# Kernel optimization log

Measured on AMD Instinct MI355X. Metric: run time of the kernel, lower is better.

The kernel has to match this reference:

```python
import jax, jax.numpy as jnp
import numpy as np

STD = 0.01

def setup_inputs() -> dict:
    key = jax.random.key(0)
    k1, k2, k3 = jax.random.split(key, 3)
    B, T, D = 16, 4096, 512
    x = jax.random.normal(k1, (B, T, D), dtype=jnp.float32)
    att_W = jax.random.normal(k2, (D, D), dtype=jnp.float32) * STD
    att_v = jax.random.normal(k3, (D,), dtype=jnp.float32) * STD
    return {"x": x, "att_W": att_W, "att_v": att_v}

def reference(x, att_W, att_v):
    # additive attention scores: tanh(x @ W) @ v -> [B, T]
    y = jnp.tanh(jnp.einsum('btd,de->bte', x, att_W))
    scores = jnp.einsum('btd,d->bt', y, att_v)
    weights = jax.nn.softmax(scores, axis=-1)          # softmax over sequence
    out = jnp.einsum('bt,btd->bd', weights, x)         # weighted sum pooling
    return out.astype(jnp.float32)
```

## Files before the change

### kernel.cpp

```cpp
#include <hip/hip_runtime.h>
#include <hip/hip_bf16.h>
#include <math.h>

#define BB 16
#define TT 4096
#define DD 512
#define MM (BB*TT)

typedef __bf16 bf16x8 __attribute__((ext_vector_type(8)));
typedef float  f32x4  __attribute__((ext_vector_type(4)));

__device__ inline unsigned short f2bf(float f) {
    unsigned u = __builtin_bit_cast(unsigned, f) + 0x8000u;
    return (unsigned short)(u >> 16);
}

__device__ inline unsigned pack_bf16x2(float lo, float hi) {
    unsigned u0 = __builtin_bit_cast(unsigned, lo) + 0x8000u;
    unsigned u1 = __builtin_bit_cast(unsigned, hi) + 0x8000u;
    return __builtin_amdgcn_perm(u1, u0, 0x07060302);
}

__device__ inline float tanh_fast(float y) {
    float e = __expf(2.0f * y);
    return 1.0f - 2.0f * __builtin_amdgcn_rcpf(e + 1.0f);
}

__global__ void wb_kernel(const float* __restrict__ W, unsigned short* __restrict__ Wb) {
    int u = blockIdx.x * 256 + threadIdx.x;
    int lane = u & 63;
    int fid  = u >> 6;
    int ni = fid & 1;
    int s  = (fid >> 1) & 15;
    int p  = (fid >> 5) & 7;
    int h  = fid >> 8;
    int n  = h * 256 + p * 32 + ni * 16 + (lane & 15);
    int k0 = s * 32 + (lane >> 4) * 8;
    unsigned short o[8];
    #pragma unroll
    for (int j = 0; j < 8; j++) o[j] = f2bf(W[(size_t)(k0 + j) * DD + n]);
    *(uint4*)(Wb + (size_t)u * 8) = *(uint4*)o;
}

__global__ __launch_bounds__(512, 2) void scorepool_kernel(
        const float* __restrict__ x, const unsigned short* __restrict__ Wb,
        const float* __restrict__ v,
        float* __restrict__ num_ws, float* __restrict__ mz_ws) {
    __shared__ unsigned short As[64 * DD];
    __shared__ float sbuf[4][64];
    __shared__ float ew[64];
    __shared__ float mzsh[2];
    __shared__ float psum[4][DD];

    const int tid  = threadIdx.x;
    const int m0   = blockIdx.x * 64;
    const int wid  = tid >> 6;
    const int lane = tid & 63;
    const int l15  = lane & 15;
    const int q    = lane >> 4;
    const int r3   = l15 & 7;
    const int wr   = (wid & 1) * 32;
    const int wh   = wid >> 1;

    #pragma unroll 4
    for (int i = 0; i < 8; i++) {
        int u = i * 512 + tid;
        int r = u >> 6;
        int c = u & 63;
        const float* gp = x + (size_t)(m0 + r) * DD + c * 8;
        f32x4 f0 = __builtin_nontemporal_load((const f32x4*)(gp));
        f32x4 f1 = __builtin_nontemporal_load((const f32x4*)(gp + 4));
        uint4 o;
        o.x = pack_bf16x2(f0.x, f0.y);
        o.y = pack_bf16x2(f0.z, f0.w);
        o.z = pack_bf16x2(f1.x, f1.y);
        o.w = pack_bf16x2(f1.z, f1.w);
        *(uint4*)(&As[r * DD + (c ^ (r & 7)) * 8]) = o;
    }

    const unsigned short* bqp = Wb + (size_t)wh * 65536 + lane * 8;
    bf16x8 b[4][2];
    #pragma unroll
    for (int g = 0; g < 3; g++) {
        b[g][0] = *(const bf16x8*)(bqp);
        b[g][1] = *(const bf16x8*)(bqp + 512);
        bqp += 1024;
    }

    __syncthreads();

    float vpart[2][4];
    #pragma unroll
    for (int mi = 0; mi < 2; mi++)
        #pragma unroll
        for (int rr = 0; rr < 4; rr++)
            vpart[mi][rr] = 0.f;

#define A_FRAG(mi, s) (*(const bf16x8*)(&As[(wr + (mi)*16 + l15) * DD + ((((s)*4 + q) ^ r3) * 8)]))

    bf16x8 a[4][2];
    #pragma unroll
    for (int g = 0; g < 3; g++) {
        a[g][0] = A_FRAG(0, g);
        a[g][1] = A_FRAG(1, g);
    }

    #pragma unroll 1
    for (int p = 0; p < 4; p++) {
        f32x4 acc[2][2];
        #pragma unroll
        for (int mi = 0; mi < 2; mi++)
            #pragma unroll
            for (int ni = 0; ni < 2; ni++)
                acc[mi][ni] = (f32x4){0.f, 0.f, 0.f, 0.f};

        #pragma unroll
        for (int s = 0; s < 16; s++) {
            const int ns = (s + 3) & 15;
            a[(s + 3) & 3][0] = A_FRAG(0, ns);
            a[(s + 3) & 3][1] = A_FRAG(1, ns);
            b[(s + 3) & 3][0] = *(const bf16x8*)(bqp);
            b[(s + 3) & 3][1] = *(const bf16x8*)(bqp + 512);
            bqp += 1024;
            #pragma unroll
            for (int mi = 0; mi < 2; mi++)
                #pragma unroll
                for (int ni = 0; ni < 2; ni++)
                    acc[mi][ni] = __builtin_amdgcn_mfma_f32_16x16x32_bf16(
                        a[s & 3][mi], b[s & 3][ni], acc[mi][ni], 0, 0, 0);
        }

        float vv0 = v[wh * 128 + p * 32 + l15];
        float vv1 = v[wh * 128 + p * 32 + 16 + l15];
        #pragma unroll
        for (int mi = 0; mi < 2; mi++)
            #pragma unroll
            for (int rr = 0; rr < 4; rr++)
                vpart[mi][rr] += tanh_fast(acc[mi][0][rr]) * vv0
                               + tanh_fast(acc[mi][1][rr]) * vv1;
    }
#undef A_FRAG

    #pragma unroll
    for (int mi = 0; mi < 2; mi++)
        #pragma unroll
        for (int rr = 0; rr < 4; rr++) {
            float sum = vpart[mi][rr];
            sum += __shfl_xor(sum, 1);
            sum += __shfl_xor(sum, 2);
            sum += __shfl_xor(sum, 4);
            sum += __shfl_xor(sum, 8);
            if (l15 == 0)
                sbuf[wh][wr + mi * 16 + q * 4 + rr] = sum;
        }
    __syncthreads();

    if (tid < 64) {
        float s = sbuf[0][tid] + sbuf[1][tid] + sbuf[2][tid] + sbuf[3][tid];
        float m = s;
        #pragma unroll
        for (int off = 32; off; off >>= 1) m = fmaxf(m, __shfl_xor(m, off));
        float e = __expf(s - m);
        float z = e;
        #pragma unroll
        for (int off = 32; off; off >>= 1) z += __shfl_xor(z, off);
        ew[tid] = e;
        if (tid == 0) { mzsh[0] = m; mzsh[1] = z; }
    }
    __syncthreads();

    const int cx = tid & 63;
    const int rg = tid >> 6;
    if (tid < 256) {
        float nacc[8];
        #pragma unroll
        for (int j = 0; j < 8; j++) nacc[j] = 0.f;
        #pragma unroll 4
        for (int i = 0; i < 16; i++) {
            int r = rg * 16 + i;
            uint4 u = *(const uint4*)(&As[r * DD + ((cx ^ (r & 7)) * 8)]);
            float e = ew[r];
            nacc[0] += e * __builtin_bit_cast(float, u.x << 16);
            nacc[1] += e * __builtin_bit_cast(float, u.x & 0xFFFF0000u);
            nacc[2] += e * __builtin_bit_cast(float, u.y << 16);
            nacc[3] += e * __builtin_bit_cast(float, u.y & 0xFFFF0000u);
            nacc[4] += e * __builtin_bit_cast(float, u.z << 16);
            nacc[5] += e * __builtin_bit_cast(float, u.z & 0xFFFF0000u);
            nacc[6] += e * __builtin_bit_cast(float, u.w << 16);
            nacc[7] += e * __builtin_bit_cast(float, u.w & 0xFFFF0000u);
        }
        *(float4*)(&psum[rg][cx * 8])     = *(float4*)(&nacc[0]);
        *(float4*)(&psum[rg][cx * 8 + 4]) = *(float4*)(&nacc[4]);
    }
    __syncthreads();

    if (tid < 128) {
        int c = tid * 4;
        f32x4 f = *(const f32x4*)(&psum[0][c]);
        f += *(const f32x4*)(&psum[1][c]);
        f += *(const f32x4*)(&psum[2][c]);
        f += *(const f32x4*)(&psum[3][c]);
        __builtin_nontemporal_store(f, (f32x4*)(num_ws + (size_t)blockIdx.x * DD + c));
    }
    if (tid == 0) {
        mz_ws[2 * blockIdx.x]     = mzsh[0];
        mz_ws[2 * blockIdx.x + 1] = mzsh[1];
    }
}

__global__ void combine_kernel(const float* __restrict__ num_ws,
                               const float* __restrict__ mz_ws,
                               float* __restrict__ out) {
    __shared__ float fs[64];
    __shared__ float sinv_sh;
    const int b   = blockIdx.x;
    const int tid = threadIdx.x;

    if (tid < 64) {
        float m = mz_ws[(b * 64 + tid) * 2];
        float z = mz_ws[(b * 64 + tid) * 2 + 1];
        float M = m;
        #pragma unroll
        for (int off = 32; off; off >>= 1) M = fmaxf(M, __shfl_xor(M, off));
        float f  = __expf(m - M);
        float fz = f * z;
        #pragma unroll
        for (int off = 32; off; off >>= 1) fz += __shfl_xor(fz, off);
        fs[tid] = f;
        if (tid == 0) sinv_sh = 1.0f / fz;
    }
    __syncthreads();

    float a0 = 0.f, a1 = 0.f;
    #pragma unroll 4
    for (int c = 0; c < 64; c++) {
        float f = fs[c];
        const float* np = num_ws + (size_t)(b * 64 + c) * DD;
        a0 += f * np[tid];
        a1 += f * np[tid + 256];
    }
    const float sinv = sinv_sh;
    out[b * DD + tid]       = a0 * sinv;
    out[b * DD + tid + 256] = a1 * sinv;
}

extern "C" void kernel_launch(void* const* d_in, const int* in_sizes, int n_in,
                              void* d_out, int out_size, void* d_ws, size_t ws_size,
                              hipStream_t stream) {
    (void)in_sizes; (void)n_in; (void)out_size; (void)ws_size;
    const float* x = (const float*)d_in[0];
    const float* W = (const float*)d_in[1];
    const float* v = (const float*)d_in[2];
    float* out = (float*)d_out;

    unsigned short* Wb = (unsigned short*)d_ws;
    float* num_ws      = (float*)((char*)d_ws + 512 * 1024 + 16 * 1024);
    float* mz_ws       = (float*)((char*)d_ws + 512 * 1024 + 16 * 1024 + 2 * 1024 * 1024);

    wb_kernel<<<128, 256, 0, stream>>>(W, Wb);

    scorepool_kernel<<<MM / 64, 512, 0, stream>>>(x, Wb, v, num_ws, mz_ws);

    combine_kernel<<<BB, 256, 0, stream>>>(num_ws, mz_ws, out);
}
```

Before: 251.0 us.

## Halve score-pool tile to 32 rows with 4-wave blocks and 128-chunk combine

The fused score and pooling kernel now processes 32 rows per block with 256 threads instead of 64 rows with 512 threads. Each wave covers all 32 rows for a 128-column quarter of the output, and the partial-sum and softmax steps shrink to match. The combine kernel now merges 128 chunks per batch using a cross-wave max and sum reduction, and the workspace offsets are moved. This doubles the grid and halves LDS per block so more blocks fit per CU, at the cost of each W fragment being reused across fewer rows and twice as many partials to combine.

```diff
diff --git a/kernel.cpp b/kernel.cpp
--- a/kernel.cpp
+++ b/kernel.cpp
@@ -42,29 +42,28 @@
     *(uint4*)(Wb + (size_t)u * 8) = *(uint4*)o;
 }
 
-__global__ __launch_bounds__(512, 2) void scorepool_kernel(
+__global__ __launch_bounds__(256, 4) void scorepool_kernel(
         const float* __restrict__ x, const unsigned short* __restrict__ Wb,
         const float* __restrict__ v,
         float* __restrict__ num_ws, float* __restrict__ mz_ws) {
-    __shared__ unsigned short As[64 * DD];
-    __shared__ float sbuf[4][64];
-    __shared__ float ew[64];
+    __shared__ unsigned short As[32 * DD];
+    __shared__ float sbuf[4][32];
+    __shared__ float ew[32];
     __shared__ float mzsh[2];
-    __shared__ float psum[4][DD];
+    __shared__ float psum[2][DD];
 
     const int tid  = threadIdx.x;
-    const int m0   = blockIdx.x * 64;
+    const int m0   = blockIdx.x * 32;
     const int wid  = tid >> 6;
     const int lane = tid & 63;
     const int l15  = lane & 15;
     const int q    = lane >> 4;
     const int r3   = l15 & 7;
-    const int wr   = (wid & 1) * 32;
-    const int wh   = wid >> 1;
+    const int wh   = wid;
 
     #pragma unroll 4
     for (int i = 0; i < 8; i++) {
-        int u = i * 512 + tid;
+        int u = i * 256 + tid;
         int r = u >> 6;
         int c = u & 63;
         const float* gp = x + (size_t)(m0 + r) * DD + c * 8;
@@ -96,7 +95,7 @@
         for (int rr = 0; rr < 4; rr++)
             vpart[mi][rr] = 0.f;
 
-#define A_FRAG(mi, s) (*(const bf16x8*)(&As[(wr + (mi)*16 + l15) * DD + ((((s)*4 + q) ^ r3) * 8)]))
+#define A_FRAG(mi, s) (*(const bf16x8*)(&As[((mi)*16 + l15) * DD + ((((s)*4 + q) ^ r3) * 8)]))
 
     bf16x8 a[4][2];
     #pragma unroll
@@ -151,19 +150,19 @@
             sum += __shfl_xor(sum, 4);
             sum += __shfl_xor(sum, 8);
             if (l15 == 0)
-                sbuf[wh][wr + mi * 16 + q * 4 + rr] = sum;
+                sbuf[wh][mi * 16 + q * 4 + rr] = sum;
         }
     __syncthreads();
 
-    if (tid < 64) {
+    if (tid < 32) {
         float s = sbuf[0][tid] + sbuf[1][tid] + sbuf[2][tid] + sbuf[3][tid];
         float m = s;
         #pragma unroll
-        for (int off = 32; off; off >>= 1) m = fmaxf(m, __shfl_xor(m, off));
+        for (int off = 16; off; off >>= 1) m = fmaxf(m, __shfl_xor(m, off));
         float e = __expf(s - m);
         float z = e;
         #pragma unroll
-        for (int off = 32; off; off >>= 1) z += __shfl_xor(z, off);
+        for (int off = 16; off; off >>= 1) z += __shfl_xor(z, off);
         ew[tid] = e;
         if (tid == 0) { mzsh[0] = m; mzsh[1] = z; }
     }
@@ -171,7 +170,7 @@
 
     const int cx = tid & 63;
     const int rg = tid >> 6;
-    if (tid < 256) {
+    if (tid < 128) {
         float nacc[8];
         #pragma unroll
         for (int j = 0; j < 8; j++) nacc[j] = 0.f;
@@ -198,8 +197,6 @@
         int c = tid * 4;
         f32x4 f = *(const f32x4*)(&psum[0][c]);
         f += *(const f32x4*)(&psum[1][c]);
-        f += *(const f32x4*)(&psum[2][c]);
-        f += *(const f32x4*)(&psum[3][c]);
         __builtin_nontemporal_store(f, (f32x4*)(num_ws + (size_t)blockIdx.x * DD + c));
     }
     if (tid == 0) {
@@ -211,35 +208,41 @@
 __global__ void combine_kernel(const float* __restrict__ num_ws,
                                const float* __restrict__ mz_ws,
                                float* __restrict__ out) {
-    __shared__ float fs[64];
-    __shared__ float sinv_sh;
+    __shared__ float red[4];
+    __shared__ float red2[4];
+    __shared__ float fs[128];
     const int b   = blockIdx.x;
     const int tid = threadIdx.x;
 
-    if (tid < 64) {
-        float m = mz_ws[(b * 64 + tid) * 2];
-        float z = mz_ws[(b * 64 + tid) * 2 + 1];
-        float M = m;
-        #pragma unroll
-        for (int off = 32; off; off >>= 1) M = fmaxf(M, __shfl_xor(M, off));
-        float f  = __expf(m - M);
-        float fz = f * z;
-        #pragma unroll
-        for (int off = 32; off; off >>= 1) fz += __shfl_xor(fz, off);
-        fs[tid] = f;
-        if (tid == 0) sinv_sh = 1.0f / fz;
-    }
-    __syncthreads();
+    float m = -1e30f, z = 0.f;
+    if (tid < 128) {
+        m = mz_ws[(b * 128 + tid) * 2];
+        z = mz_ws[(b * 128 + tid) * 2 + 1];
+    }
+    float M = m;
+    #pragma unroll
+    for (int off = 32; off; off >>= 1) M = fmaxf(M, __shfl_xor(M, off));
+    if ((tid & 63) == 0) red[tid >> 6] = M;
+    __syncthreads();
+    M = fmaxf(fmaxf(red[0], red[1]), fmaxf(red[2], red[3]));
+
+    float f  = (tid < 128) ? __expf(m - M) : 0.f;
+    float fz = f * z;
+    #pragma unroll
+    for (int off = 32; off; off >>= 1) fz += __shfl_xor(fz, off);
+    if ((tid & 63) == 0) red2[tid >> 6] = fz;
+    if (tid < 128) fs[tid] = f;
+    __syncthreads();
+    const float sinv = 1.0f / (red2[0] + red2[1] + red2[2] + red2[3]);
 
     float a0 = 0.f, a1 = 0.f;
     #pragma unroll 4
-    for (int c = 0; c < 64; c++) {
-        float f = fs[c];
-        const float* np = num_ws + (size_t)(b * 64 + c) * DD;
-        a0 += f * np[tid];
-        a1 += f * np[tid + 256];
-    }
-    const float sinv = sinv_sh;
+    for (int c = 0; c < 128; c++) {
+        float fc = fs[c];
+        const float* np = num_ws + (size_t)(b * 128 + c) * DD;
+        a0 += fc * np[tid];
+        a1 += fc * np[tid + 256];
+    }
     out[b * DD + tid]       = a0 * sinv;
     out[b * DD + tid + 256] = a1 * sinv;
 }
@@ -255,11 +258,11 @@
 
     unsigned short* Wb = (unsigned short*)d_ws;
     float* num_ws      = (float*)((char*)d_ws + 512 * 1024 + 16 * 1024);
-    float* mz_ws       = (float*)((char*)d_ws + 512 * 1024 + 16 * 1024 + 2 * 1024 * 1024);
+    float* mz_ws       = (float*)((char*)d_ws + 512 * 1024 + 16 * 1024 + 4 * 1024 * 1024);
 
     wb_kernel<<<128, 256, 0, stream>>>(W, Wb);
 
-    scorepool_kernel<<<MM / 64, 512, 0, stream>>>(x, Wb, v, num_ws, mz_ws);
+    scorepool_kernel<<<MM / 32, 256, 0, stream>>>(x, Wb, v, num_ws, mz_ws);
 
     combine_kernel<<<BB, 256, 0, stream>>>(num_ws, mz_ws, out);
 }
```

Measured after the change: 334.1 us. 33.1% more time.

## Halve scorepool block to 256 threads with 64-row warp tiles

Applied to the files above, without the earlier changes.

The scorepool kernel now runs 4 waves per block instead of 8, and each wave covers all 64 rows against its 128-column slice of W, so every B fragment loaded from global feeds twice as many MFMAs. The A-fragment prefetch depth drops from 3 stages to 2 to keep register use in check. Score partials are reduced per p-iteration straight into shared memory instead of being held in registers. The goal is less W traffic per row, paid for with fewer waves to hide latency, a heavier register load, and more shuffle and shared-memory work inside the loop.

```diff
diff --git a/kernel.cpp b/kernel.cpp
--- a/kernel.cpp
+++ b/kernel.cpp
@@ -42,7 +42,7 @@
     *(uint4*)(Wb + (size_t)u * 8) = *(uint4*)o;
 }
 
-__global__ __launch_bounds__(512, 2) void scorepool_kernel(
+__global__ __launch_bounds__(256, 2) void scorepool_kernel(
         const float* __restrict__ x, const unsigned short* __restrict__ Wb,
         const float* __restrict__ v,
         float* __restrict__ num_ws, float* __restrict__ mz_ws) {
@@ -59,12 +59,13 @@
     const int l15  = lane & 15;
     const int q    = lane >> 4;
     const int r3   = l15 & 7;
-    const int wr   = (wid & 1) * 32;
-    const int wh   = wid >> 1;
+    const int wh   = wid;
+
+    ((float*)sbuf)[tid] = 0.f;
 
     #pragma unroll 4
-    for (int i = 0; i < 8; i++) {
-        int u = i * 512 + tid;
+    for (int i = 0; i < 16; i++) {
+        int u = i * 256 + tid;
         int r = u >> 6;
         int c = u & 63;
         const float* gp = x + (size_t)(m0 + r) * DD + c * 8;
@@ -89,70 +90,55 @@
 
     __syncthreads();
 
-    float vpart[2][4];
-    #pragma unroll
-    for (int mi = 0; mi < 2; mi++)
-        #pragma unroll
-        for (int rr = 0; rr < 4; rr++)
-            vpart[mi][rr] = 0.f;
-
-#define A_FRAG(mi, s) (*(const bf16x8*)(&As[(wr + (mi)*16 + l15) * DD + ((((s)*4 + q) ^ r3) * 8)]))
-
-    bf16x8 a[4][2];
-    #pragma unroll
-    for (int g = 0; g < 3; g++) {
-        a[g][0] = A_FRAG(0, g);
-        a[g][1] = A_FRAG(1, g);
-    }
+#define A_FRAG(mi, s) (*(const bf16x8*)(&As[((mi)*16 + l15) * DD + ((((s)*4 + q) ^ r3) * 8)]))
+
+    bf16x8 a[2][4];
+    #pragma unroll
+    for (int mi = 0; mi < 4; mi++) a[0][mi] = A_FRAG(mi, 0);
 
     #pragma unroll 1
     for (int p = 0; p < 4; p++) {
-        f32x4 acc[2][2];
-        #pragma unroll
-        for (int mi = 0; mi < 2; mi++)
+        f32x4 acc[4][2];
+        #pragma unroll
+        for (int mi = 0; mi < 4; mi++) {
+            acc[mi][0] = (f32x4){0.f, 0.f, 0.f, 0.f};
+            acc[mi][1] = (f32x4){0.f, 0.f, 0.f, 0.f};
+        }
+
+        #pragma unroll
+        for (int s = 0; s < 16; s++) {
+            const int ns = (s + 1) & 15;
             #pragma unroll
-            for (int ni = 0; ni < 2; ni++)
-                acc[mi][ni] = (f32x4){0.f, 0.f, 0.f, 0.f};
-
-        #pragma unroll
-        for (int s = 0; s < 16; s++) {
-            const int ns = (s + 3) & 15;
-            a[(s + 3) & 3][0] = A_FRAG(0, ns);
-            a[(s + 3) & 3][1] = A_FRAG(1, ns);
+            for (int mi = 0; mi < 4; mi++) a[(s + 1) & 1][mi] = A_FRAG(mi, ns);
             b[(s + 3) & 3][0] = *(const bf16x8*)(bqp);
             b[(s + 3) & 3][1] = *(const bf16x8*)(bqp + 512);
             bqp += 1024;
             #pragma unroll
-            for (int mi = 0; mi < 2; mi++)
+            for (int mi = 0; mi < 4; mi++)
                 #pragma unroll
                 for (int ni = 0; ni < 2; ni++)
                     acc[mi][ni] = __builtin_amdgcn_mfma_f32_16x16x32_bf16(
-                        a[s & 3][mi], b[s & 3][ni], acc[mi][ni], 0, 0, 0);
+                        a[s & 1][mi], b[s & 3][ni], acc[mi][ni], 0, 0, 0);
         }
 
         float vv0 = v[wh * 128 + p * 32 + l15];
         float vv1 = v[wh * 128 + p * 32 + 16 + l15];
         #pragma unroll
-        for (int mi = 0; mi < 2; mi++)
+        for (int mi = 0; mi < 4; mi++)
             #pragma unroll
-            for (int rr = 0; rr < 4; rr++)
-                vpart[mi][rr] += tanh_fast(acc[mi][0][rr]) * vv0
-                               + tanh_fast(acc[mi][1][rr]) * vv1;
+            for (int rr = 0; rr < 4; rr++) {
+                float sum = tanh_fast(acc[mi][0][rr]) * vv0
+                          + tanh_fast(acc[mi][1][rr]) * vv1;
+                sum += __shfl_xor(sum, 1);
+                sum += __shfl_xor(sum, 2);
+                sum += __shfl_xor(sum, 4);
+                sum += __shfl_xor(sum, 8);
+                if (l15 == 0)
+                    sbuf[wh][mi * 16 + q * 4 + rr] += sum;
+            }
     }
 #undef A_FRAG
 
-    #pragma unroll
-    for (int mi = 0; mi < 2; mi++)
-        #pragma unroll
-        for (int rr = 0; rr < 4; rr++) {
-            float sum = vpart[mi][rr];
-            sum += __shfl_xor(sum, 1);
-            sum += __shfl_xor(sum, 2);
-            sum += __shfl_xor(sum, 4);
-            sum += __shfl_xor(sum, 8);
-            if (l15 == 0)
-                sbuf[wh][wr + mi * 16 + q * 4 + rr] = sum;
-        }
     __syncthreads();
 
     if (tid < 64) {
@@ -171,27 +157,25 @@
 
     const int cx = tid & 63;
     const int rg = tid >> 6;
-    if (tid < 256) {
-        float nacc[8];
-        #pragma unroll
-        for (int j = 0; j < 8; j++) nacc[j] = 0.f;
-        #pragma unroll 4
-        for (int i = 0; i < 16; i++) {
-            int r = rg * 16 + i;
-            uint4 u = *(const uint4*)(&As[r * DD + ((cx ^ (r & 7)) * 8)]);
-            float e = ew[r];
-            nacc[0] += e * __builtin_bit_cast(float, u.x << 16);
-            nacc[1] += e * __builtin_bit_cast(float, u.x & 0xFFFF0000u);
-            nacc[2] += e * __builtin_bit_cast(float, u.y << 16);
-            nacc[3] += e * __builtin_bit_cast(float, u.y & 0xFFFF0000u);
-            nacc[4] += e * __builtin_bit_cast(float, u.z << 16);
-            nacc[5] += e * __builtin_bit_cast(float, u.z & 0xFFFF0000u);
-            nacc[6] += e * __builtin_bit_cast(float, u.w << 16);
-            nacc[7] += e * __builtin_bit_cast(float, u.w & 0xFFFF0000u);
-        }
-        *(float4*)(&psum[rg][cx * 8])     = *(float4*)(&nacc[0]);
-        *(float4*)(&psum[rg][cx * 8 + 4]) = *(float4*)(&nacc[4]);
-    }
+    float nacc[8];
+    #pragma unroll
+    for (int j = 0; j < 8; j++) nacc[j] = 0.f;
+    #pragma unroll 4
+    for (int i = 0; i < 16; i++) {
+        int r = rg * 16 + i;
+        uint4 u = *(const uint4*)(&As[r * DD + ((cx ^ (r & 7)) * 8)]);
+        float e = ew[r];
+        nacc[0] += e * __builtin_bit_cast(float, u.x << 16);
+        nacc[1] += e * __builtin_bit_cast(float, u.x & 0xFFFF0000u);
+        nacc[2] += e * __builtin_bit_cast(float, u.y << 16);
+        nacc[3] += e * __builtin_bit_cast(float, u.y & 0xFFFF0000u);
+        nacc[4] += e * __builtin_bit_cast(float, u.z << 16);
+        nacc[5] += e * __builtin_bit_cast(float, u.z & 0xFFFF0000u);
+        nacc[6] += e * __builtin_bit_cast(float, u.w << 16);
+        nacc[7] += e * __builtin_bit_cast(float, u.w & 0xFFFF0000u);
+    }
+    *(float4*)(&psum[rg][cx * 8])     = *(float4*)(&nacc[0]);
+    *(float4*)(&psum[rg][cx * 8 + 4]) = *(float4*)(&nacc[4]);
     __syncthreads();
 
     if (tid < 128) {
@@ -259,7 +243,7 @@
 
     wb_kernel<<<128, 256, 0, stream>>>(W, Wb);
 
-    scorepool_kernel<<<MM / 64, 512, 0, stream>>>(x, Wb, v, num_ws, mz_ws);
+    scorepool_kernel<<<MM / 64, 256, 0, stream>>>(x, Wb, v, num_ws, mz_ws);
 
     combine_kernel<<<BB, 256, 0, stream>>>(num_ws, mz_ws, out);
 }
```

New measurement: 301.6 us. 20.1% more time.
